# Optimization experiments

Measured on AMD Instinct MI355X. Metric: run time of the kernel, lower is better.

The kernel has to match this reference:

```python
import jax, jax.numpy as jnp
import numpy as np

H = 1024   # hidden_dim
V = 32000  # vocab_size
L = 256    # sequence length


def setup_inputs() -> dict:
    key = jax.random.key(0)
    ks = jax.random.split(key, 12)
    s = 0.02
    rn = lambda k, shape: jax.random.normal(k, shape, jnp.float32) * s
    return dict(
        input_seq=jax.random.randint(ks[0], (L,), 0, V),
        embeds=rn(ks[1], (V, H)),
        enc_Wih=rn(ks[2], (4 * H, H)), enc_Whh=rn(ks[3], (4 * H, H)),
        enc_bih=jnp.zeros(4 * H, jnp.float32), enc_bhh=jnp.zeros(4 * H, jnp.float32),
        dec_Wih=rn(ks[4], (4 * H, 2 * H)), dec_Whh=rn(ks[5], (4 * H, H)),
        dec_bih=jnp.zeros(4 * H, jnp.float32), dec_bhh=jnp.zeros(4 * H, jnp.float32),
        out_W=rn(ks[6], (V, H)), out_b=jnp.zeros(V, jnp.float32),
        v=jax.random.uniform(ks[7], (H,), jnp.float32) * 0.05,
        w1=jax.random.uniform(ks[8], (H, H), jnp.float32) * 0.05,
        w2=jax.random.uniform(ks[9], (H, H), jnp.float32) * 0.05,
    )


def _lstm_cell(x, h, c, Wih, Whh, bih, bhh):
    # PyTorch LSTM gate order: i, f, g, o
    g = Wih @ x + bih + Whh @ h + bhh
    i, f, gg, o = jnp.split(g, 4)
    i, f, o = jax.nn.sigmoid(i), jax.nn.sigmoid(f), jax.nn.sigmoid(o)
    c_new = f * c + i * jnp.tanh(gg)
    h_new = o * jnp.tanh(c_new)
    return h_new, c_new


def reference(input_seq, embeds, enc_Wih, enc_Whh, enc_bih, enc_bhh,
              dec_Wih, dec_Whh, dec_bih, dec_bhh, out_W, out_b, v, w1, w2):
    x_emb = embeds[input_seq]  # (L, H)

    # --- encoder LSTM (batch=1, seq-major) ---
    def enc_step(carry, x):
        h, c = carry
        h, c = _lstm_cell(x, h, c, enc_Wih, enc_Whh, enc_bih, enc_bhh)
        return (h, c), h

    h0 = jnp.zeros(H, jnp.float32)
    (h, c), E = jax.lax.scan(enc_step, (h0, h0), x_emb)  # E: (L, H)

    # additive attention: score_i = v . tanh(w1 @ h + w2 @ e_i)
    # precompute E @ w2^T once (same math as recomputing each step)
    Ew2 = E @ w2.T  # (L, H)

    def dec_step(carry, _):
        h, c, prev = carry
        prev_r = jax.nn.relu(prev)                       # relu on prev embedding
        scores = jnp.tanh(w1 @ h + Ew2) @ v              # (L,)
        a = jax.nn.softmax(scores)
        ctx = a @ E                                      # (H,)
        xin = jnp.concatenate([prev_r, ctx])             # (2H,)
        h2, c2 = _lstm_cell(xin, h, c, dec_Wih, dec_Whh, dec_bih, dec_bhh)
        logits = out_W @ h2 + out_b                      # (V,)
        idx = jnp.argmax(logits)
        return (h2, c2, embeds[idx]), (logits, idx)

    _, (preds, seq) = jax.lax.scan(dec_step, (h, c, jnp.zeros(H, jnp.float32)),
                                   None, length=L)
    return preds, seq  # (L, V) logits, (L,) predicted ids
```

## Files before the change

kernel.cpp:

```cpp
#include <hip/hip_runtime.h>
#include <math.h>


#define H   1024
#define V   32000
#define L   256
#define NB  256
#define NT  512
#define NW  (NT/64)
#define MARGIN 2e-4f

typedef unsigned long long u64;

__device__ __forceinline__ float wsum(float v){
  #pragma unroll
  for (int off = 32; off > 0; off >>= 1) v += __shfl_down(v, off, 64);
  return v;
}
__device__ __forceinline__ float wmaxf(float v){
  #pragma unroll
  for (int off = 32; off > 0; off >>= 1) v = fmaxf(v, __shfl_down(v, off, 64));
  return v;
}
__device__ __forceinline__ u64 wmaxu(u64 v){
  #pragma unroll
  for (int off = 32; off > 0; off >>= 1){
    u64 o = __shfl_down(v, off, 64);
    if (o > v) v = o;
  }
  return v;
}
__device__ __forceinline__ float sigmoidf(float x){ return 1.f/(1.f+expf(-x)); }
__device__ __forceinline__ unsigned fkey(float f){
  unsigned u = __float_as_uint(f);
  return (u & 0x80000000u) ? ~u : (u | 0x80000000u);
}
__device__ __forceinline__ float unfkey(unsigned k){
  unsigned u = (k & 0x80000000u) ? (k & 0x7FFFFFFFu) : ~k;
  return __uint_as_float(u);
}
__device__ __forceinline__ float dotp(const float* __restrict__ Wr,
                                      const float4* __restrict__ x4, int lane){
  const float4* w4 = (const float4*)Wr;
  float s = 0.f;
  #pragma unroll
  for (int u = 0; u < 4; ++u){
    float4 a = w4[lane + 64*u];
    float4 x = x4[lane + 64*u];
    s += a.x*x.x + a.y*x.y + a.z*x.z + a.w*x.w;
  }
  return s;
}
__device__ __forceinline__ float bdot8(uint4 q, float4 ha, float4 hb){
  float s;
  s  = __uint_as_float(q.x << 16)         * ha.x;
  s += __uint_as_float(q.x & 0xFFFF0000u) * ha.y;
  s += __uint_as_float(q.y << 16)         * ha.z;
  s += __uint_as_float(q.y & 0xFFFF0000u) * ha.w;
  s += __uint_as_float(q.z << 16)         * hb.x;
  s += __uint_as_float(q.z & 0xFFFF0000u) * hb.y;
  s += __uint_as_float(q.w << 16)         * hb.z;
  s += __uint_as_float(q.w & 0xFFFF0000u) * hb.w;
  return s;
}

__device__ __forceinline__ void ow_issue(const float* __restrict__ outW,
                                         int r0, int w, int lane, int g,
                                         float* dst){
  #pragma unroll
  for (int rr2 = 0; rr2 < 2; ++rr2){
    const int k  = w*16 + g*2 + rr2;
    const int kc = (k > 124) ? 124 : k;
    const float* src = outW + (size_t)(r0 + kc)*H + lane*4;
    #pragma unroll
    for (int kk = 0; kk < 4; ++kk){
      __builtin_amdgcn_global_load_lds(
          (const __attribute__((address_space(1))) unsigned int*)(src + kk*256),
          (__attribute__((address_space(3))) unsigned int*)(dst + rr2*H + kk*256),
          16, 0, 0);
    }
  }
}
__device__ __forceinline__ void owh_issue(const unsigned short* __restrict__ owbf,
                                          int r0, int w, int lane, int g,
                                          unsigned short* dst){
  #pragma unroll
  for (int rr2 = 0; rr2 < 2; ++rr2){
    const int k  = w*16 + g*2 + rr2;
    const int kc = (k > 124) ? 124 : k;
    const unsigned short* src = owbf + (size_t)(r0 + kc)*H + lane*8;
    #pragma unroll
    for (int kk = 0; kk < 2; ++kk){
      __builtin_amdgcn_global_load_lds(
          (const __attribute__((address_space(1))) unsigned int*)(src + kk*512),
          (__attribute__((address_space(3))) unsigned int*)(dst + rr2*1024 + kk*512),
          16, 0, 0);
    }
  }
}

__device__ __forceinline__ void pub(u64* ch, int idx, unsigned tag, float f){
  u64 v = ((u64)tag << 32) | (u64)__float_as_uint(f);
  __hip_atomic_store(ch + idx, v, __ATOMIC_RELAXED, __HIP_MEMORY_SCOPE_AGENT);
}
__device__ __forceinline__ float spin1(u64* p, unsigned tag){
  u64 v = __hip_atomic_load(p, __ATOMIC_RELAXED, __HIP_MEMORY_SCOPE_AGENT);
  while ((unsigned)(v >> 32) != tag){
    __builtin_amdgcn_s_sleep(2);
    v = __hip_atomic_load(p, __ATOMIC_RELAXED, __HIP_MEMORY_SCOPE_AGENT);
  }
  return __uint_as_float((unsigned)v);
}
__device__ __forceinline__ void ch_read(u64* ch, unsigned tag, float* dst, int tid){
  u64 v0 = __hip_atomic_load(ch + tid,      __ATOMIC_RELAXED, __HIP_MEMORY_SCOPE_AGENT);
  u64 v1 = __hip_atomic_load(ch + tid + NT, __ATOMIC_RELAXED, __HIP_MEMORY_SCOPE_AGENT);
  while ((unsigned)(v0 >> 32) != tag){
    __builtin_amdgcn_s_sleep(2);
    v0 = __hip_atomic_load(ch + tid, __ATOMIC_RELAXED, __HIP_MEMORY_SCOPE_AGENT);
  }
  while ((unsigned)(v1 >> 32) != tag){
    __builtin_amdgcn_s_sleep(2);
    v1 = __hip_atomic_load(ch + tid + NT, __ATOMIC_RELAXED, __HIP_MEMORY_SCOPE_AGENT);
  }
  dst[tid]      = __uint_as_float((unsigned)v0);
  dst[tid + NT] = __uint_as_float((unsigned)v1);
}
__device__ __forceinline__ unsigned win_reduce(u64* slot, unsigned tag,
                                               u64* s_k, unsigned* s_w,
                                               int tid, int w, int lane){
  u64 key = 0ull;
  if (tid < NB){
    u64* p = slot + tid;
    u64 v = __hip_atomic_load(p, __ATOMIC_RELAXED, __HIP_MEMORY_SCOPE_AGENT);
    while ((unsigned)(v >> 47) != tag){
      __builtin_amdgcn_s_sleep(2);
      v = __hip_atomic_load(p, __ATOMIC_RELAXED, __HIP_MEMORY_SCOPE_AGENT);
    }
    key = v & 0x7FFFFFFFFFFFull;
  }
  key = wmaxu(key);
  if (lane == 0) s_k[w] = key;
  __syncthreads();
  if (tid == 0){
    u64 m = s_k[0];
    for (int k = 1; k < NW; ++k) if (s_k[k] > m) m = s_k[k];
    *s_w = 0x7FFFu - (unsigned)(m & 0x7FFFull);
  }
  __syncthreads();
  return *s_w;
}

__device__ __forceinline__ unsigned resolve_winner(
    unsigned T, u64* chWinP, u64* chWin2,
    const float* __restrict__ outW, const float* sB,
    const float* s_logf, const float* s_ob,
    u64* s_wk, u64* s_k, float* s_bv, int* s_bi, u64* s_m12,
    int* s_nc, int* s_cr, unsigned* s_widx,
    int b, int tid, int w, int lane)
{
  const int pb = (int)(T & 1u);
  u64* pair = chWinP + pb*2*NB;
  {
    u64 v = __hip_atomic_load(pair + tid, __ATOMIC_RELAXED, __HIP_MEMORY_SCOPE_AGENT);
    while ((unsigned)(v >> 47) != T){
      __builtin_amdgcn_s_sleep(2);
      v = __hip_atomic_load(pair + tid, __ATOMIC_RELAXED, __HIP_MEMORY_SCOPE_AGENT);
    }
    s_wk[tid] = v & 0x7FFFFFFFFFFFull;
  }
  __syncthreads();
  u64 a = (tid < NB) ? s_wk[2*tid] : 0ull;
  a = wmaxu(a);
  if (lane == 0) s_k[w] = a;
  __syncthreads();
  if (tid == 0){
    u64 m = s_k[0];
    for (int k = 1; k < NW; ++k) if (s_k[k] > m) m = s_k[k];
    s_m12[0] = m;
  }
  __syncthreads();
  const u64 m1 = s_m12[0];
  const unsigned widx1 = 0x7FFFu - (unsigned)(m1 & 0x7FFFull);
  const int beta = (int)(widx1 / 125u);
  u64 c = (tid < NB) ? ((tid == beta) ? s_wk[2*tid+1] : s_wk[2*tid]) : 0ull;
  c = wmaxu(c);
  if (lane == 0) s_k[w] = c;
  __syncthreads();
  if (tid == 0){
    u64 m = s_k[0];
    for (int k = 1; k < NW; ++k) if (s_k[k] > m) m = s_k[k];
    s_m12[1] = m;
  }
  __syncthreads();
  const float f1 = unfkey((unsigned)(m1 >> 15));
  const float f2 = unfkey((unsigned)(s_m12[1] >> 15));
  if (f1 - f2 >= MARGIN) return widx1;

  if (tid == 0) *s_nc = 0;
  __syncthreads();
  const float thr = f1 - MARGIN;
  if (tid < 125 && s_logf[tid] >= thr){
    int sl = atomicAdd(s_nc, 1);
    if (sl < 16) s_cr[sl] = tid;
  }
  __syncthreads();
  const int nc = min(*s_nc, 16);
  float cv = -INFINITY; int ci = 0x7FFFFFFF;
  for (int q = w; q < nc; q += NW){
    const int lr = s_cr[q];
    float s = wsum(dotp(outW + (size_t)(b*125 + lr)*H, (const float4*)sB, lane));
    if (lane == 0){
      const float dv = s + s_ob[lr];
      const int gr = b*125 + lr;
      if (dv > cv || (dv == cv && gr < ci)){ cv = dv; ci = gr; }
    }
  }
  if (lane == 0){ s_bv[w] = cv; s_bi[w] = ci; }
  __syncthreads();
  if (tid == 0){
    float v0 = -INFINITY; int i0 = 0x7FFFFFFF;
    for (int k = 0; k < NW; ++k){
      if (s_bv[k] > v0 || (s_bv[k] == v0 && s_bi[k] < i0)){ v0 = s_bv[k]; i0 = s_bi[k]; }
    }
    const u64 pk = ((u64)T << 47) | ((u64)fkey(v0) << 15)
                 | (u64)(0x7FFFu - ((unsigned)i0 & 0x7FFFu));
    __hip_atomic_store(chWin2 + pb*NB + b, pk,
                       __ATOMIC_RELAXED, __HIP_MEMORY_SCOPE_AGENT);
  }
  __syncthreads();
  return win_reduce(chWin2 + pb*NB, T, s_k, s_widx, tid, w, lane);
}

__global__ __launch_bounds__(NT, 1) void seq2seq_fused_bf16(
    const int*   __restrict__ seq_in, const float* __restrict__ embeds,
    const float* __restrict__ eWih,   const float* __restrict__ eWhh,
    const float* __restrict__ ebih,   const float* __restrict__ ebhh,
    const float* __restrict__ dWih,   const float* __restrict__ dWhh,
    const float* __restrict__ dbih,   const float* __restrict__ dbhh,
    const float* __restrict__ outW,   const float* __restrict__ outb,
    const float* __restrict__ vvec,   const float* __restrict__ w1,
    const float* __restrict__ w2,
    float* __restrict__ out, u64* __restrict__ ws,
    const unsigned short* __restrict__ owbf)
{
  const int b = blockIdx.x, tid = threadIdx.x;
  const int w = tid >> 6, lane = tid & 63;
  const int j0 = b * 4;

  u64* chH  = ws;
  u64* chW1 = ws + 2*H;
  u64* chSc = ws + 4*H;
  u64* chCx = ws + 4*H + 2*NB;
  u64* chH2 = ws + 6*H + 2*NB;
  u64* chWinP = ws + 8*H + 2*NB;
  u64* chWin2 = ws + 8*H + 6*NB;

  __shared__ __align__(16) float sA[H];
  __shared__ __align__(16) float sB[H];
  __shared__ __align__(16) float sMyE[H];
  __shared__ __align__(16) float sEw2[H];
  __shared__ __align__(16) float sEcol[L*4];
  __shared__ __align__(16) unsigned short sOWh[NW][2][2048];
  __shared__ __align__(16) float sV[H];
  __shared__ __align__(16) u64 s_wk[NT];
  __shared__ float s_logf[128];
  __shared__ float s_ob[128];
  __shared__ float s_gate[16], s_gpart[16], s_c[4];
  __shared__ float s_redA[NW], s_red4[NW][4];
  __shared__ float s_bv[NW], s_bv2[NW];
  __shared__ int   s_bi[NW];
  __shared__ float s_bcast[2];
  __shared__ u64   s_k[NW];
  __shared__ u64   s_m12[2];
  __shared__ int   s_nc, s_cr[16];
  __shared__ unsigned s_widx;

  if (tid < 4) s_c[tid] = 0.f;
  for (int i = tid; i < H; i += NT) sV[i] = vvec[i];
  if (tid < 128) s_ob[tid] = outb[b*125 + ((tid > 124) ? 124 : tid)];

  for (int t = 0; t < L; ++t){
    if (t == 0){
      for (int i = tid; i < H; i += NT) sB[i] = 0.f;
    } else {
      ch_read(chH + (t & 1)*H, (unsigned)t, sB, tid);
    }
    if (t == b + 1){ sMyE[tid] = sB[tid]; sMyE[tid + NT] = sB[tid + NT]; }
    const int tok = seq_in[t];
    for (int i = tid; i < H; i += NT) sA[i] = embeds[(size_t)tok*H + i];
    __syncthreads();
    const float4* x4 = (const float4*)sA;
    const float4* h4 = (const float4*)sB;
    #pragma unroll
    for (int q2 = 0; q2 < 2; ++q2){
      const int lr = w + q2*NW;
      const int r  = (lr >> 2)*H + j0 + (lr & 3);
      float s = dotp(eWih + (size_t)r*H, x4, lane)
              + dotp(eWhh + (size_t)r*H, h4, lane);
      s = wsum(s);
      if (lane == 0) s_gate[lr] = s + ebih[r] + ebhh[r];
    }
    __syncthreads();
    if (tid < 4){
      const float ig = sigmoidf(s_gate[tid]);
      const float fg = sigmoidf(s_gate[4 + tid]);
      const float gg = tanhf   (s_gate[8 + tid]);
      const float og = sigmoidf(s_gate[12 + tid]);
      const float c  = fg*s_c[tid] + ig*gg;
      const float hn = og*tanhf(c);
      s_c[tid] = c;
      sEcol[t*4 + tid] = hn;
      pub(chH + ((t+1) & 1)*H, j0 + tid, (unsigned)(t+1), hn);
    }
  }
  if (b == L-1) ch_read(chH + ((L & 1))*H, (unsigned)L, sMyE, tid);
  __syncthreads();

  {
    const float4* e4p = (const float4*)sMyE;
    for (int g4 = 0; g4 < 32; ++g4){
      const int jr = w*128 + g4*4;
      const float4* W0 = (const float4*)(w2 + (size_t)(jr+0)*H);
      const float4* W1 = (const float4*)(w2 + (size_t)(jr+1)*H);
      const float4* W2 = (const float4*)(w2 + (size_t)(jr+2)*H);
      const float4* W3 = (const float4*)(w2 + (size_t)(jr+3)*H);
      float s0=0, s1=0, s2=0, s3=0;
      #pragma unroll
      for (int u = 0; u < 4; ++u){
        const float4 e = e4p[lane + 64*u];
        float4 a0 = W0[lane+64*u]; s0 += a0.x*e.x+a0.y*e.y+a0.z*e.z+a0.w*e.w;
        float4 a1 = W1[lane+64*u]; s1 += a1.x*e.x+a1.y*e.y+a1.z*e.z+a1.w*e.w;
        float4 a2 = W2[lane+64*u]; s2 += a2.x*e.x+a2.y*e.y+a2.z*e.z+a2.w*e.w;
        float4 a3 = W3[lane+64*u]; s3 += a3.x*e.x+a3.y*e.y+a3.z*e.z+a3.w*e.w;
      }
      s0 = wsum(s0); s1 = wsum(s1); s2 = wsum(s2); s3 = wsum(s3);
      if (lane == 0){ sEw2[jr]=s0; sEw2[jr+1]=s1; sEw2[jr+2]=s2; sEw2[jr+3]=s3; }
    }
  }
  __syncthreads();

  ch_read(chH + (L & 1)*H, (unsigned)L, sB, tid);
  __syncthreads();
  {
    const float4* hh4 = (const float4*)sB;
    #pragma unroll
    for (int q2 = 0; q2 < 2; ++q2){
      const int lr = w + q2*NW;
      const int r  = (lr >> 2)*H + j0 + (lr & 3);
      float s = wsum(dotp(dWhh + (size_t)r*H, hh4, lane));
      if (lane == 0) s_gpart[lr] = s + dbih[r] + dbhh[r];
    }
    if (w < 4){
      const int r = j0 + w;
      float s = wsum(dotp(w1 + (size_t)r*H, hh4, lane));
      if (lane == 0) pub(chW1 + 0*H, r, 1u, s);
    }
  }

  for (int t = 0; t < L; ++t){
    unsigned widx = 0u;
    if (t > 0){
      widx = resolve_winner((unsigned)t, chWinP, chWin2, outW, sB,
                            s_logf, s_ob, s_wk, s_k, s_bv, s_bi, s_m12,
                            &s_nc, s_cr, &s_widx, b, tid, w, lane);
      if (b == 0 && tid == 0)
        __builtin_nontemporal_store((float)widx, out + (size_t)L*V + (t-1));
      for (int i = tid; i < H; i += NT)
        sA[i] = fmaxf(embeds[(size_t)widx*H + i], 0.f);
      __syncthreads();
      const float4* pr4 = (const float4*)sA;
      #pragma unroll
      for (int q2 = 0; q2 < 2; ++q2){
        const int lr = w + q2*NW;
        const int r  = (lr >> 2)*H + j0 + (lr & 3);
        float s = wsum(dotp(dWih + (size_t)r*2*H, pr4, lane));
        if (lane == 0) s_gpart[lr] += s;
      }
    }
    owh_issue(owbf, b*125, w, lane, 0, &sOWh[w][0][0]);
    owh_issue(owbf, b*125, w, lane, 1, &sOWh[w][1][0]);

    __syncthreads();
    ch_read(chW1 + (t & 1)*H, (unsigned)(t+1), sA, tid);
    __syncthreads();
    {
      float p = 0.f;
      for (int i = tid; i < H; i += NT) p += sV[i]*tanhf(sA[i] + sEw2[i]);
      p = wsum(p);
      if (lane == 0) s_redA[w] = p;
      __syncthreads();
      if (tid == 0){
        float s = 0.f;
        for (int k = 0; k < NW; ++k) s += s_redA[k];
        pub(chSc + (t & 1)*NB, b, (unsigned)(t+1), s);
      }
    }

    __syncthreads();
    {
      float sv = -INFINITY;
      if (tid < L) sv = spin1(chSc + (t & 1)*NB + tid, (unsigned)(t+1));
      float mx = wmaxf(sv);
      if (lane == 0) s_redA[w] = mx;
      __syncthreads();
      if (tid == 0){
        float m = s_redA[0];
        for (int k = 1; k < NW; ++k) m = fmaxf(m, s_redA[k]);
        s_bcast[0] = m;
      }
      __syncthreads();
      const float m = s_bcast[0];
      float e = (tid < L) ? expf(sv - m) : 0.f;
      float ss = wsum(e);
      if (lane == 0) s_redA[w] = ss;
      __syncthreads();
      if (tid == 0){
        float s = 0.f;
        for (int k = 0; k < NW; ++k) s += s_redA[k];
        s_bcast[1] = s;
      }
      __syncthreads();
      const float a = e / s_bcast[1];
      float qx = 0, qy = 0, qz = 0, qw = 0;
      if (tid < L){
        const float4 ev = *(const float4*)(sEcol + tid*4);
        qx = a*ev.x; qy = a*ev.y; qz = a*ev.z; qw = a*ev.w;
      }
      qx = wsum(qx); qy = wsum(qy); qz = wsum(qz); qw = wsum(qw);
      if (lane == 0){ s_red4[w][0]=qx; s_red4[w][1]=qy; s_red4[w][2]=qz; s_red4[w][3]=qw; }
      __syncthreads();
      if (tid < 4){
        float s = 0.f;
        for (int k = 0; k < NW; ++k) s += s_red4[k][tid];
        pub(chCx + (t & 1)*H, j0 + tid, (unsigned)(t+1), s);
      }
    }

    ch_read(chCx + (t & 1)*H, (unsigned)(t+1), sA, tid);
    __syncthreads();
    const float4* cx4 = (const float4*)sA;
    #pragma unroll
    for (int q2 = 0; q2 < 2; ++q2){
      const int lr = w + q2*NW;
      const int r  = (lr >> 2)*H + j0 + (lr & 3);
      float s = wsum(dotp(dWih + (size_t)r*2*H + H, cx4, lane));
      if (lane == 0) s_gate[lr] = s_gpart[lr] + s;
    }
    __syncthreads();
    if (tid < 4){
      const float ig = sigmoidf(s_gate[tid]);
      const float fg = sigmoidf(s_gate[4 + tid]);
      const float gg = tanhf   (s_gate[8 + tid]);
      const float og = sigmoidf(s_gate[12 + tid]);
      const float c  = fg*s_c[tid] + ig*gg;
      const float hn = og*tanhf(c);
      s_c[tid] = c;
      pub(chH2 + ((t+1) & 1)*H, j0 + tid, (unsigned)(t+1), hn);
    }

    ch_read(chH2 + ((t+1) & 1)*H, (unsigned)(t+1), sB, tid);
    __syncthreads();
    {
      const float4* h4b = (const float4*)sB;
      const float4 hA0 = h4b[2*lane],     hA1 = h4b[2*lane+1];
      const float4 hB0 = h4b[128+2*lane], hB1 = h4b[128+2*lane+1];
      float bv1 = -INFINITY, bv2 = -INFINITY; int bi1 = 0x7FFFFFFF;
      const int r0 = b * 125;

#define EB_GROUP(G, WSTR)                                                      \
      {                                                                        \
        asm volatile("s_waitcnt vmcnt(" WSTR ")" ::: "memory");                \
        const uint4* rq = (const uint4*)&sOWh[w][(G)&1][0];                    \
        const uint4 q0 = rq[lane],     q1 = rq[lane+64];                       \
        const uint4 q2 = rq[lane+128], q3 = rq[lane+192];                      \
        float s0 = bdot8(q0, hA0, hA1) + bdot8(q1, hB0, hB1);                  \
        float s1 = bdot8(q2, hA0, hA1) + bdot8(q3, hB0, hB1);                  \
        if ((G) < 6) owh_issue(owbf, r0, w, lane, (G)+2, &sOWh[w][(G)&1][0]);  \
        s0 = wsum(s0); s1 = wsum(s1);                                          \
        if (lane == 0){                                                        \
          const int k0 = w*16 + (G)*2;                                         \
          const float d0 = s0 + s_ob[k0], d1 = s1 + s_ob[k0+1];                \
          s_logf[k0] = d0; s_logf[k0+1] = d1;                                  \
          if (k0 <= 124){                                                      \
            if (d0 > bv1 || (d0 == bv1 && r0+k0 < bi1)){ bv2=bv1; bv1=d0; bi1=r0+k0; } \
            else if (d0 > bv2) bv2 = d0;                                       \
          }                                                                    \
          if (k0+1 <= 124){                                                    \
            if (d1 > bv1 || (d1 == bv1 && r0+k0+1 < bi1)){ bv2=bv1; bv1=d1; bi1=r0+k0+1; } \
            else if (d1 > bv2) bv2 = d1;                                       \
          }                                                                    \
        }                                                                      \
      }

      EB_GROUP(0, "0")
      EB_GROUP(1, "4")
      EB_GROUP(2, "4")
      EB_GROUP(3, "4")
      EB_GROUP(4, "4")
      EB_GROUP(5, "4")
      EB_GROUP(6, "4")
      EB_GROUP(7, "0")
#undef EB_GROUP

      if (lane == 0){ s_bv[w] = bv1; s_bi[w] = bi1; s_bv2[w] = bv2; }
      __syncthreads();
      if (tid == 0){
        float v1 = -INFINITY, v2 = -INFINITY; int i1 = 0x7FFFFFFF, aw = 0;
        for (int k = 0; k < NW; ++k){
          if (s_bv[k] > v1 || (s_bv[k] == v1 && s_bi[k] < i1)){ v1 = s_bv[k]; i1 = s_bi[k]; aw = k; }
        }
        for (int k = 0; k < NW; ++k){
          const float cc = (k == aw) ? s_bv2[k] : s_bv[k];
          if (cc > v2) v2 = cc;
        }
        const u64 k1 = ((u64)(unsigned)(t+1) << 47) | ((u64)fkey(v1) << 15)
                     | (u64)(0x7FFFu - ((unsigned)i1 & 0x7FFFu));
        const u64 k2 = ((u64)(unsigned)(t+1) << 47) | ((u64)fkey(v2) << 15);
        u64* pr = chWinP + ((t+1) & 1)*2*NB + 2*b;
        __hip_atomic_store(pr,     k1, __ATOMIC_RELAXED, __HIP_MEMORY_SCOPE_AGENT);
        __hip_atomic_store(pr + 1, k2, __ATOMIC_RELAXED, __HIP_MEMORY_SCOPE_AGENT);
      }
      if (tid < 125)
        __builtin_nontemporal_store(s_logf[tid], out + (size_t)t*V + r0 + tid);

      const float4* hh4 = (const float4*)sB;
      if (w < 4){
        const int r = j0 + w;
        float s = wsum(dotp(w1 + (size_t)r*H, hh4, lane));
        if (lane == 0) pub(chW1 + ((t+1) & 1)*H, r, (unsigned)(t+2), s);
      }
      #pragma unroll
      for (int q2i = 0; q2i < 2; ++q2i){
        const int lr = w + q2i*NW;
        const int r  = (lr >> 2)*H + j0 + (lr & 3);
        float s = wsum(dotp(dWhh + (size_t)r*H, hh4, lane));
        if (lane == 0) s_gpart[lr] = s + dbih[r] + dbhh[r];
      }
    }
  }

  {
    unsigned widx = resolve_winner((unsigned)L, chWinP, chWin2, outW, sB,
                                   s_logf, s_ob, s_wk, s_k, s_bv, s_bi, s_m12,
                                   &s_nc, s_cr, &s_widx, b, tid, w, lane);
    if (b == 0 && tid == 0)
      __builtin_nontemporal_store((float)widx, out + (size_t)L*V + (L-1));
  }
}

__global__ __launch_bounds__(NT, 1) void seq2seq_fused_f32(
    const int*   __restrict__ seq_in, const float* __restrict__ embeds,
    const float* __restrict__ eWih,   const float* __restrict__ eWhh,
    const float* __restrict__ ebih,   const float* __restrict__ ebhh,
    const float* __restrict__ dWih,   const float* __restrict__ dWhh,
    const float* __restrict__ dbih,   const float* __restrict__ dbhh,
    const float* __restrict__ outW,   const float* __restrict__ outb,
    const float* __restrict__ vvec,   const float* __restrict__ w1,
    const float* __restrict__ w2,
    float* __restrict__ out, u64* __restrict__ ws)
{
  const int b = blockIdx.x, tid = threadIdx.x;
  const int w = tid >> 6, lane = tid & 63;
  const int j0 = b * 4;

  u64* chH  = ws;
  u64* chW1 = ws + 2*H;
  u64* chSc = ws + 4*H;
  u64* chCx = ws + 4*H + 2*NB;
  u64* chH2 = ws + 6*H + 2*NB;
  u64* chWin= ws + 8*H + 2*NB;

  __shared__ __align__(16) float sA[H];
  __shared__ __align__(16) float sB[H];
  __shared__ __align__(16) float sMyE[H];
  __shared__ __align__(16) float sEw2[H];
  __shared__ __align__(16) float sEcol[L*4];
  __shared__ __align__(16) float sOW[NW][2][2*H];
  __shared__ __align__(16) float sV[H];
  __shared__ float s_logf[128];
  __shared__ float s_ob[128];
  __shared__ float s_gate[16], s_gpart[16], s_c[4];
  __shared__ float s_redA[NW], s_red4[NW][4];
  __shared__ float s_bv[NW];
  __shared__ int   s_bi[NW];
  __shared__ float s_bcast[2];
  __shared__ u64   s_k[NW];
  __shared__ unsigned s_widx;

  if (tid < 4) s_c[tid] = 0.f;
  for (int i = tid; i < H; i += NT) sV[i] = vvec[i];
  if (tid < 128) s_ob[tid] = outb[b*125 + ((tid > 124) ? 124 : tid)];

  for (int t = 0; t < L; ++t){
    if (t == 0){
      for (int i = tid; i < H; i += NT) sB[i] = 0.f;
    } else {
      ch_read(chH + (t & 1)*H, (unsigned)t, sB, tid);
    }
    if (t == b + 1){ sMyE[tid] = sB[tid]; sMyE[tid + NT] = sB[tid + NT]; }
    const int tok = seq_in[t];
    for (int i = tid; i < H; i += NT) sA[i] = embeds[(size_t)tok*H + i];
    __syncthreads();
    const float4* x4 = (const float4*)sA;
    const float4* h4 = (const float4*)sB;
    #pragma unroll
    for (int q2 = 0; q2 < 2; ++q2){
      const int lr = w + q2*NW;
      const int r  = (lr >> 2)*H + j0 + (lr & 3);
      float s = dotp(eWih + (size_t)r*H, x4, lane)
              + dotp(eWhh + (size_t)r*H, h4, lane);
      s = wsum(s);
      if (lane == 0) s_gate[lr] = s + ebih[r] + ebhh[r];
    }
    __syncthreads();
    if (tid < 4){
      const float ig = sigmoidf(s_gate[tid]);
      const float fg = sigmoidf(s_gate[4 + tid]);
      const float gg = tanhf   (s_gate[8 + tid]);
      const float og = sigmoidf(s_gate[12 + tid]);
      const float c  = fg*s_c[tid] + ig*gg;
      const float hn = og*tanhf(c);
      s_c[tid] = c;
      sEcol[t*4 + tid] = hn;
      pub(chH + ((t+1) & 1)*H, j0 + tid, (unsigned)(t+1), hn);
    }
  }
  if (b == L-1) ch_read(chH + ((L & 1))*H, (unsigned)L, sMyE, tid);
  __syncthreads();

  {
    const float4* e4p = (const float4*)sMyE;
    for (int g4 = 0; g4 < 32; ++g4){
      const int jr = w*128 + g4*4;
      const float4* W0 = (const float4*)(w2 + (size_t)(jr+0)*H);
      const float4* W1 = (const float4*)(w2 + (size_t)(jr+1)*H);
      const float4* W2 = (const float4*)(w2 + (size_t)(jr+2)*H);
      const float4* W3 = (const float4*)(w2 + (size_t)(jr+3)*H);
      float s0=0, s1=0, s2=0, s3=0;
      #pragma unroll
      for (int u = 0; u < 4; ++u){
        const float4 e = e4p[lane + 64*u];
        float4 a0 = W0[lane+64*u]; s0 += a0.x*e.x+a0.y*e.y+a0.z*e.z+a0.w*e.w;
        float4 a1 = W1[lane+64*u]; s1 += a1.x*e.x+a1.y*e.y+a1.z*e.z+a1.w*e.w;
        float4 a2 = W2[lane+64*u]; s2 += a2.x*e.x+a2.y*e.y+a2.z*e.z+a2.w*e.w;
        float4 a3 = W3[lane+64*u]; s3 += a3.x*e.x+a3.y*e.y+a3.z*e.z+a3.w*e.w;
      }
      s0 = wsum(s0); s1 = wsum(s1); s2 = wsum(s2); s3 = wsum(s3);
      if (lane == 0){ sEw2[jr]=s0; sEw2[jr+1]=s1; sEw2[jr+2]=s2; sEw2[jr+3]=s3; }
    }
  }
  __syncthreads();

  for (int t = 0; t < L; ++t){
    unsigned widx = 0u;
    if (t > 0){
      widx = win_reduce(chWin + ((t-1) & 1)*NB, (unsigned)t, s_k, &s_widx, tid, w, lane);
      if (b == 0 && tid == 0) out[(size_t)L*V + (t-1)] = (float)widx;
    }
    if (t == 0) ch_read(chH + ((L & 1))*H, (unsigned)L, sB, tid);
    for (int i = tid; i < H; i += NT){
      float pv = (t > 0) ? embeds[(size_t)widx*H + i] : 0.f;
      sA[i] = fmaxf(pv, 0.f);
    }
    __syncthreads();
    const float4* hh4 = (const float4*)sB;
    const float4* pr4 = (const float4*)sA;
    #pragma unroll
    for (int q2 = 0; q2 < 2; ++q2){
      const int lr = w + q2*NW;
      const int r  = (lr >> 2)*H + j0 + (lr & 3);
      float s = dotp(dWhh + (size_t)r*H, hh4, lane);
      if (t > 0) s += dotp(dWih + (size_t)r*2*H, pr4, lane);
      s = wsum(s);
      if (lane == 0) s_gpart[lr] = s + dbih[r] + dbhh[r];
    }
    if (w < 4){
      const int r = j0 + w;
      float s = wsum(dotp(w1 + (size_t)r*H, hh4, lane));
      if (lane == 0) pub(chW1 + (t & 1)*H, r, (unsigned)(t+1), s);
    }
    ow_issue(outW, b*125, w, lane, 0, &sOW[w][0][0]);
    ow_issue(outW, b*125, w, lane, 1, &sOW[w][1][0]);

    __syncthreads();
    ch_read(chW1 + (t & 1)*H, (unsigned)(t+1), sA, tid);
    __syncthreads();
    {
      float p = 0.f;
      for (int i = tid; i < H; i += NT) p += sV[i]*tanhf(sA[i] + sEw2[i]);
      p = wsum(p);
      if (lane == 0) s_redA[w] = p;
      __syncthreads();
      if (tid == 0){
        float s = 0.f;
        for (int k = 0; k < NW; ++k) s += s_redA[k];
        pub(chSc + (t & 1)*NB, b, (unsigned)(t+1), s);
      }
    }

// ... 181 lines not shown
```

Measured before the change: 9.455 ms.

## Warp-specialize decoder: split output-projection waves from recurrent hop waves

Splits each block's 8 waves into 4 'hop' waves that run the attention and LSTM recurrence chain and 4 waves that stream the bf16 output projection and the per-block argmax. The two groups communicate through LDS ready counters and a custom partial barrier instead of __syncthreads. The goal is to take the 32000-row vocab projection off the serial critical path: the winner resolution for step t is deferred until after the next step's attention and context work, overlapping the logits computation with that recurrence. In exchange it adds shared-memory double buffers, spin-waits inside the block and halves the waves available to each role, with risk of ordering bugs.

```diff
diff --git a/kernel.cpp b/kernel.cpp
--- a/kernel.cpp
+++ b/kernel.cpp
@@ -8,6 +8,7 @@
 #define NB  256
 #define NT  512
 #define NW  (NT/64)
+#define NHOP 4
 #define MARGIN 2e-4f
 
 typedef unsigned long long u64;
@@ -81,49 +82,75 @@
     }
   }
 }
-__device__ __forceinline__ void owh_issue(const unsigned short* __restrict__ owbf,
-                                          int r0, int w, int lane, int g,
-                                          unsigned short* dst){
+__device__ __forceinline__ void owh2_issue(const unsigned short* __restrict__ owbf,
+                                           int r0, int we, int lane, int g,
+                                           unsigned short* dst){
   #pragma unroll
-  for (int rr2 = 0; rr2 < 2; ++rr2){
-    const int k  = w*16 + g*2 + rr2;
+  for (int rr = 0; rr < 2; ++rr){
+    const int k  = we*32 + g*2 + rr;
     const int kc = (k > 124) ? 124 : k;
     const unsigned short* src = owbf + (size_t)(r0 + kc)*H + lane*8;
     #pragma unroll
     for (int kk = 0; kk < 2; ++kk){
       __builtin_amdgcn_global_load_lds(
           (const __attribute__((address_space(1))) unsigned int*)(src + kk*512),
-          (__attribute__((address_space(3))) unsigned int*)(dst + rr2*1024 + kk*512),
+          (__attribute__((address_space(3))) unsigned int*)(dst + rr*1024 + kk*512),
           16, 0, 0);
     }
   }
 }
 
+__device__ __forceinline__ u64 aload(u64* p){
+  return __hip_atomic_load(p, __ATOMIC_RELAXED, __HIP_MEMORY_SCOPE_AGENT);
+}
 __device__ __forceinline__ void pub(u64* ch, int idx, unsigned tag, float f){
   u64 v = ((u64)tag << 32) | (u64)__float_as_uint(f);
   __hip_atomic_store(ch + idx, v, __ATOMIC_RELAXED, __HIP_MEMORY_SCOPE_AGENT);
 }
 __device__ __forceinline__ float spin1(u64* p, unsigned tag){
-  u64 v = __hip_atomic_load(p, __ATOMIC_RELAXED, __HIP_MEMORY_SCOPE_AGENT);
+  u64 v = aload(p);
   while ((unsigned)(v >> 32) != tag){
     __builtin_amdgcn_s_sleep(2);
-    v = __hip_atomic_load(p, __ATOMIC_RELAXED, __HIP_MEMORY_SCOPE_AGENT);
+    v = aload(p);
   }
   return __uint_as_float((unsigned)v);
 }
+__device__ __forceinline__ u64 spin47(u64* p, unsigned tag){
+  u64 v = aload(p);
+  while ((unsigned)(v >> 47) != tag){
+    __builtin_amdgcn_s_sleep(2);
+    v = aload(p);
+  }
+  return v;
+}
 __device__ __forceinline__ void ch_read(u64* ch, unsigned tag, float* dst, int tid){
-  u64 v0 = __hip_atomic_load(ch + tid,      __ATOMIC_RELAXED, __HIP_MEMORY_SCOPE_AGENT);
-  u64 v1 = __hip_atomic_load(ch + tid + NT, __ATOMIC_RELAXED, __HIP_MEMORY_SCOPE_AGENT);
-  while ((unsigned)(v0 >> 32) != tag){
-    __builtin_amdgcn_s_sleep(2);
-    v0 = __hip_atomic_load(ch + tid, __ATOMIC_RELAXED, __HIP_MEMORY_SCOPE_AGENT);
-  }
-  while ((unsigned)(v1 >> 32) != tag){
-    __builtin_amdgcn_s_sleep(2);
-    v1 = __hip_atomic_load(ch + tid + NT, __ATOMIC_RELAXED, __HIP_MEMORY_SCOPE_AGENT);
-  }
+  u64 v0 = aload(ch + tid);
+  u64 v1 = aload(ch + tid + NT);
+  while ((unsigned)(v0 >> 32) != tag){ __builtin_amdgcn_s_sleep(2); v0 = aload(ch + tid); }
+  while ((unsigned)(v1 >> 32) != tag){ __builtin_amdgcn_s_sleep(2); v1 = aload(ch + tid + NT); }
   dst[tid]      = __uint_as_float((unsigned)v0);
   dst[tid + NT] = __uint_as_float((unsigned)v1);
+}
+__device__ __forceinline__ void ch_read4(u64* ch, unsigned tag, float* dst, int tid){
+  u64 v[4];
+  #pragma unroll
+  for (int k = 0; k < 4; ++k) v[k] = aload(ch + tid + k*256);
+  #pragma unroll
+  for (int k = 0; k < 4; ++k){
+    while ((unsigned)(v[k] >> 32) != tag){
+      __builtin_amdgcn_s_sleep(2);
+      v[k] = aload(ch + tid + k*256);
+    }
+  }
+  #pragma unroll
+  for (int k = 0; k < 4; ++k) dst[tid + k*256] = __uint_as_float((unsigned)v[k]);
+}
+__device__ __forceinline__ void hbar(int* c, int& ep, int lane){
+  ep += NHOP;
+  if (lane == 0)
+    __hip_atomic_fetch_add(c, 1, __ATOMIC_RELEASE, __HIP_MEMORY_SCOPE_WORKGROUP);
+  while (__hip_atomic_load(c, __ATOMIC_ACQUIRE, __HIP_MEMORY_SCOPE_WORKGROUP) < ep)
+    __builtin_amdgcn_s_sleep(1);
 }
 __device__ __forceinline__ unsigned win_reduce(u64* slot, unsigned tag,
                                                u64* s_k, unsigned* s_w,
@@ -131,11 +158,8 @@
   u64 key = 0ull;
   if (tid < NB){
     u64* p = slot + tid;
-    u64 v = __hip_atomic_load(p, __ATOMIC_RELAXED, __HIP_MEMORY_SCOPE_AGENT);
-    while ((unsigned)(v >> 47) != tag){
-      __builtin_amdgcn_s_sleep(2);
-      v = __hip_atomic_load(p, __ATOMIC_RELAXED, __HIP_MEMORY_SCOPE_AGENT);
-    }
+    u64 v = aload(p);
+    while ((unsigned)(v >> 47) != tag){ __builtin_amdgcn_s_sleep(2); v = aload(p); }
     key = v & 0x7FFFFFFFFFFFull;
   }
   key = wmaxu(key);
@@ -148,87 +172,6 @@
   }
   __syncthreads();
   return *s_w;
-}
-
-__device__ __forceinline__ unsigned resolve_winner(
-    unsigned T, u64* chWinP, u64* chWin2,
-    const float* __restrict__ outW, const float* sB,
-    const float* s_logf, const float* s_ob,
-    u64* s_wk, u64* s_k, float* s_bv, int* s_bi, u64* s_m12,
-    int* s_nc, int* s_cr, unsigned* s_widx,
-    int b, int tid, int w, int lane)
-{
-  const int pb = (int)(T & 1u);
-  u64* pair = chWinP + pb*2*NB;
-  {
-    u64 v = __hip_atomic_load(pair + tid, __ATOMIC_RELAXED, __HIP_MEMORY_SCOPE_AGENT);
-    while ((unsigned)(v >> 47) != T){
-      __builtin_amdgcn_s_sleep(2);
-      v = __hip_atomic_load(pair + tid, __ATOMIC_RELAXED, __HIP_MEMORY_SCOPE_AGENT);
-    }
-    s_wk[tid] = v & 0x7FFFFFFFFFFFull;
-  }
-  __syncthreads();
-  u64 a = (tid < NB) ? s_wk[2*tid] : 0ull;
-  a = wmaxu(a);
-  if (lane == 0) s_k[w] = a;
-  __syncthreads();
-  if (tid == 0){
-    u64 m = s_k[0];
-    for (int k = 1; k < NW; ++k) if (s_k[k] > m) m = s_k[k];
-    s_m12[0] = m;
-  }
-  __syncthreads();
-  const u64 m1 = s_m12[0];
-  const unsigned widx1 = 0x7FFFu - (unsigned)(m1 & 0x7FFFull);
-  const int beta = (int)(widx1 / 125u);
-  u64 c = (tid < NB) ? ((tid == beta) ? s_wk[2*tid+1] : s_wk[2*tid]) : 0ull;
-  c = wmaxu(c);
-  if (lane == 0) s_k[w] = c;
-  __syncthreads();
-  if (tid == 0){
-    u64 m = s_k[0];
-    for (int k = 1; k < NW; ++k) if (s_k[k] > m) m = s_k[k];
-    s_m12[1] = m;
-  }
-  __syncthreads();
-  const float f1 = unfkey((unsigned)(m1 >> 15));
-  const float f2 = unfkey((unsigned)(s_m12[1] >> 15));
-  if (f1 - f2 >= MARGIN) return widx1;
-
-  if (tid == 0) *s_nc = 0;
-  __syncthreads();
-  const float thr = f1 - MARGIN;
-  if (tid < 125 && s_logf[tid] >= thr){
-    int sl = atomicAdd(s_nc, 1);
-    if (sl < 16) s_cr[sl] = tid;
-  }
-  __syncthreads();
-  const int nc = min(*s_nc, 16);
-  float cv = -INFINITY; int ci = 0x7FFFFFFF;
-  for (int q = w; q < nc; q += NW){
-    const int lr = s_cr[q];
-    float s = wsum(dotp(outW + (size_t)(b*125 + lr)*H, (const float4*)sB, lane));
-    if (lane == 0){
-      const float dv = s + s_ob[lr];
-      const int gr = b*125 + lr;
-      if (dv > cv || (dv == cv && gr < ci)){ cv = dv; ci = gr; }
-    }
-  }
-  if (lane == 0){ s_bv[w] = cv; s_bi[w] = ci; }
-  __syncthreads();
-  if (tid == 0){
-    float v0 = -INFINITY; int i0 = 0x7FFFFFFF;
-    for (int k = 0; k < NW; ++k){
-      if (s_bv[k] > v0 || (s_bv[k] == v0 && s_bi[k] < i0)){ v0 = s_bv[k]; i0 = s_bi[k]; }
-    }
-    const u64 pk = ((u64)T << 47) | ((u64)fkey(v0) << 15)
-                 | (u64)(0x7FFFu - ((unsigned)i0 & 0x7FFFu));
-    __hip_atomic_store(chWin2 + pb*NB + b, pk,
-                       __ATOMIC_RELAXED, __HIP_MEMORY_SCOPE_AGENT);
-  }
-  __syncthreads();
-  return win_reduce(chWin2 + pb*NB, T, s_k, s_widx, tid, w, lane);
 }
 
 __global__ __launch_bounds__(NT, 1) void seq2seq_fused_bf16(
@@ -247,11 +190,11 @@
   const int w = tid >> 6, lane = tid & 63;
   const int j0 = b * 4;
 
-  u64* chH  = ws;
-  u64* chW1 = ws + 2*H;
-  u64* chSc = ws + 4*H;
-  u64* chCx = ws + 4*H + 2*NB;
-  u64* chH2 = ws + 6*H + 2*NB;
+  u64* chH    = ws;
+  u64* chW1   = ws + 2*H;
+  u64* chSc   = ws + 4*H;
+  u64* chCx   = ws + 4*H + 2*NB;
+  u64* chH2   = ws + 6*H + 2*NB;
   u64* chWinP = ws + 8*H + 2*NB;
   u64* chWin2 = ws + 8*H + 6*NB;
 
@@ -260,22 +203,28 @@
   __shared__ __align__(16) float sMyE[H];
   __shared__ __align__(16) float sEw2[H];
   __shared__ __align__(16) float sEcol[L*4];
-  __shared__ __align__(16) unsigned short sOWh[NW][2][2048];
+  __shared__ __align__(16) unsigned short sOWh[4][2][2048];
   __shared__ __align__(16) float sV[H];
-  __shared__ __align__(16) u64 s_wk[NT];
+  __shared__ __align__(16) float sH2[2][H];
+  __shared__ __align__(16) float sCtx[H];
+  __shared__ __align__(16) float sPr[H];
   __shared__ float s_logf[128];
   __shared__ float s_ob[128];
   __shared__ float s_gate[16], s_gpart[16], s_c[4];
-  __shared__ float s_redA[NW], s_red4[NW][4];
-  __shared__ float s_bv[NW], s_bv2[NW];
-  __shared__ int   s_bi[NW];
-  __shared__ float s_bcast[2];
-  __shared__ u64   s_k[NW];
-  __shared__ u64   s_m12[2];
+  __shared__ float s_redA[8], s_red4[8][4];
+  __shared__ float s_bv[8];
+  __shared__ int   s_bi[8];
+  __shared__ float s_ebv1[4], s_ebv2[4];
+  __shared__ int   s_ebi[4];
+  __shared__ int   s_ewdone[4];
+  __shared__ int   s_h2rdy;
+  __shared__ int   s_hb;
+  __shared__ u64   s_k[8];
   __shared__ int   s_nc, s_cr[16];
-  __shared__ unsigned s_widx;
 
   if (tid < 4) s_c[tid] = 0.f;
+  if (tid < 4) s_ewdone[tid] = 0;
+  if (tid == 0){ s_h2rdy = 0; s_hb = 0; }
   for (int i = tid; i < H; i += NT) sV[i] = vvec[i];
   if (tid < 128) s_ob[tid] = outb[b*125 + ((tid > 124) ? 124 : tid)];
 
@@ -339,10 +288,10 @@
   }
   __syncthreads();
 
-  ch_read(chH + (L & 1)*H, (unsigned)L, sB, tid);
+  ch_read(chH + (L & 1)*H, (unsigned)L, sH2[0], tid);
   __syncthreads();
   {
-    const float4* hh4 = (const float4*)sB;
+    const float4* hh4 = (const float4*)sH2[0];
     #pragma unroll
     for (int q2 = 0; q2 < 2; ++q2){
       const int lr = w + q2*NW;
@@ -356,129 +305,34 @@
       if (lane == 0) pub(chW1 + 0*H, r, 1u, s);
     }
   }
-
-  for (int t = 0; t < L; ++t){
-    unsigned widx = 0u;
-    if (t > 0){
-      widx = resolve_winner((unsigned)t, chWinP, chWin2, outW, sB,
-                            s_logf, s_ob, s_wk, s_k, s_bv, s_bi, s_m12,
-                            &s_nc, s_cr, &s_widx, b, tid, w, lane);
-      if (b == 0 && tid == 0)
-        __builtin_nontemporal_store((float)widx, out + (size_t)L*V + (t-1));
-      for (int i = tid; i < H; i += NT)
-        sA[i] = fmaxf(embeds[(size_t)widx*H + i], 0.f);
-      __syncthreads();
-      const float4* pr4 = (const float4*)sA;
-      #pragma unroll
-      for (int q2 = 0; q2 < 2; ++q2){
-        const int lr = w + q2*NW;
-        const int r  = (lr >> 2)*H + j0 + (lr & 3);
-        float s = wsum(dotp(dWih + (size_t)r*2*H, pr4, lane));
-        if (lane == 0) s_gpart[lr] += s;
-      }
-    }
-    owh_issue(owbf, b*125, w, lane, 0, &sOWh[w][0][0]);
-    owh_issue(owbf, b*125, w, lane, 1, &sOWh[w][1][0]);
-
-    __syncthreads();
-    ch_read(chW1 + (t & 1)*H, (unsigned)(t+1), sA, tid);
-    __syncthreads();
-    {
-      float p = 0.f;
-      for (int i = tid; i < H; i += NT) p += sV[i]*tanhf(sA[i] + sEw2[i]);
-      p = wsum(p);
-      if (lane == 0) s_redA[w] = p;
-      __syncthreads();
-      if (tid == 0){
-        float s = 0.f;
-        for (int k = 0; k < NW; ++k) s += s_redA[k];
-        pub(chSc + (t & 1)*NB, b, (unsigned)(t+1), s);
-      }
-    }
-
-    __syncthreads();
-    {
-      float sv = -INFINITY;
-      if (tid < L) sv = spin1(chSc + (t & 1)*NB + tid, (unsigned)(t+1));
-      float mx = wmaxf(sv);
-      if (lane == 0) s_redA[w] = mx;
-      __syncthreads();
-      if (tid == 0){
-        float m = s_redA[0];
-        for (int k = 1; k < NW; ++k) m = fmaxf(m, s_redA[k]);
-        s_bcast[0] = m;
-      }
-      __syncthreads();
-      const float m = s_bcast[0];
-      float e = (tid < L) ? expf(sv - m) : 0.f;
-      float ss = wsum(e);
-      if (lane == 0) s_redA[w] = ss;
-      __syncthreads();
-      if (tid == 0){
-        float s = 0.f;
-        for (int k = 0; k < NW; ++k) s += s_redA[k];
-        s_bcast[1] = s;
-      }
-      __syncthreads();
-      const float a = e / s_bcast[1];
-      float qx = 0, qy = 0, qz = 0, qw = 0;
-      if (tid < L){
-        const float4 ev = *(const float4*)(sEcol + tid*4);
-        qx = a*ev.x; qy = a*ev.y; qz = a*ev.z; qw = a*ev.w;
-      }
-      qx = wsum(qx); qy = wsum(qy); qz = wsum(qz); qw = wsum(qw);
-      if (lane == 0){ s_red4[w][0]=qx; s_red4[w][1]=qy; s_red4[w][2]=qz; s_red4[w][3]=qw; }
-      __syncthreads();
-      if (tid < 4){
-        float s = 0.f;
-        for (int k = 0; k < NW; ++k) s += s_red4[k][tid];
-        pub(chCx + (t & 1)*H, j0 + tid, (unsigned)(t+1), s);
-      }
-    }
-
-    ch_read(chCx + (t & 1)*H, (unsigned)(t+1), sA, tid);
-    __syncthreads();
-    const float4* cx4 = (const float4*)sA;
-    #pragma unroll
-    for (int q2 = 0; q2 < 2; ++q2){
-      const int lr = w + q2*NW;
-      const int r  = (lr >> 2)*H + j0 + (lr & 3);
-      float s = wsum(dotp(dWih + (size_t)r*2*H + H, cx4, lane));
-      if (lane == 0) s_gate[lr] = s_gpart[lr] + s;
-    }
-    __syncthreads();
-    if (tid < 4){
-      const float ig = sigmoidf(s_gate[tid]);
-      const float fg = sigmoidf(s_gate[4 + tid]);
-      const float gg = tanhf   (s_gate[8 + tid]);
-      const float og = sigmoidf(s_gate[12 + tid]);
-      const float c  = fg*s_c[tid] + ig*gg;
-      const float hn = og*tanhf(c);
-      s_c[tid] = c;
-      pub(chH2 + ((t+1) & 1)*H, j0 + tid, (unsigned)(t+1), hn);
-    }
-
-    ch_read(chH2 + ((t+1) & 1)*H, (unsigned)(t+1), sB, tid);
-    __syncthreads();
-    {
-      const float4* h4b = (const float4*)sB;
+  __syncthreads();
+
+  if (w >= NHOP){
+    const int we = w - NHOP;
+    const int r0 = b * 125;
+    owh2_issue(owbf, r0, we, lane, 0, &sOWh[we][0][0]);
+    owh2_issue(owbf, r0, we, lane, 1, &sOWh[we][1][0]);
+    volatile int* rdy = &s_h2rdy;
+    for (int s = 0; s < L; ++s){
+      while (*rdy < s + 1) __builtin_amdgcn_s_sleep(2);
+      __builtin_amdgcn_sched_barrier(0);
+      const float4* h4b = (const float4*)sH2[(s+1)&1];
       const float4 hA0 = h4b[2*lane],     hA1 = h4b[2*lane+1];
       const float4 hB0 = h4b[128+2*lane], hB1 = h4b[128+2*lane+1];
       float bv1 = -INFINITY, bv2 = -INFINITY; int bi1 = 0x7FFFFFFF;
-      const int r0 = b * 125;
-
-#define EB_GROUP(G, WSTR)                                                      \
+
+#define EG(G)                                                                  \
       {                                                                        \
-        asm volatile("s_waitcnt vmcnt(" WSTR ")" ::: "memory");                \
-        const uint4* rq = (const uint4*)&sOWh[w][(G)&1][0];                    \
-        const uint4 q0 = rq[lane],     q1 = rq[lane+64];                       \
-        const uint4 q2 = rq[lane+128], q3 = rq[lane+192];                      \
-        float s0 = bdot8(q0, hA0, hA1) + bdot8(q1, hB0, hB1);                  \
-        float s1 = bdot8(q2, hA0, hA1) + bdot8(q3, hB0, hB1);                  \
-        if ((G) < 6) owh_issue(owbf, r0, w, lane, (G)+2, &sOWh[w][(G)&1][0]);  \
+        asm volatile("s_waitcnt vmcnt(4)" ::: "memory");                       \
+        const uint4* rq = (const uint4*)&sOWh[we][(G)&1][0];                   \
+        const uint4 qa = rq[lane],     qb = rq[lane+64];                       \
+        const uint4 qc = rq[lane+128], qd = rq[lane+192];                      \
+        float s0 = bdot8(qa, hA0, hA1) + bdot8(qb, hB0, hB1);                  \
+        float s1 = bdot8(qc, hA0, hA1) + bdot8(qd, hB0, hB1);                  \
+        owh2_issue(owbf, r0, we, lane, ((G)+2)&15, &sOWh[we][(G)&1][0]);       \
         s0 = wsum(s0); s1 = wsum(s1);                                          \
         if (lane == 0){                                                        \
-          const int k0 = w*16 + (G)*2;                                         \
+          const int k0 = we*32 + (G)*2;                                        \
           const float d0 = s0 + s_ob[k0], d1 = s1 + s_ob[k0+1];                \
           s_logf[k0] = d0; s_logf[k0+1] = d1;                                  \
           if (k0 <= 124){                                                      \
@@ -491,60 +345,240 @@
           }                                                                    \
         }                                                                      \
       }
-
-      EB_GROUP(0, "0")
-      EB_GROUP(1, "4")
-      EB_GROUP(2, "4")
-      EB_GROUP(3, "4")
-      EB_GROUP(4, "4")
-      EB_GROUP(5, "4")
-      EB_GROUP(6, "4")
-      EB_GROUP(7, "0")
-#undef EB_GROUP
-
-      if (lane == 0){ s_bv[w] = bv1; s_bi[w] = bi1; s_bv2[w] = bv2; }
-      __syncthreads();
+      EG(0)  EG(1)  EG(2)  EG(3)  EG(4)  EG(5)  EG(6)  EG(7)
+      EG(8)  EG(9)  EG(10) EG(11) EG(12) EG(13) EG(14) EG(15)
+#undef EG
+      if (lane == 0){
+        s_ebv1[we] = bv1; s_ebv2[we] = bv2; s_ebi[we] = bi1;
+        asm volatile("s_waitcnt lgkmcnt(0)" ::: "memory");
+        *(volatile int*)&s_ewdone[we] = s + 1;
+      }
+    }
+    asm volatile("s_waitcnt vmcnt(0)" ::: "memory");
+  } else {
+    const int hw = w;
+    int ep = 0;
+
+    auto W_phase = [&](int t) -> unsigned {
+      volatile int* ed = s_ewdone;
+      while (ed[0] < t || ed[1] < t || ed[2] < t || ed[3] < t)
+        __builtin_amdgcn_s_sleep(2);
+      __builtin_amdgcn_sched_barrier(0);
       if (tid == 0){
         float v1 = -INFINITY, v2 = -INFINITY; int i1 = 0x7FFFFFFF, aw = 0;
-        for (int k = 0; k < NW; ++k){
-          if (s_bv[k] > v1 || (s_bv[k] == v1 && s_bi[k] < i1)){ v1 = s_bv[k]; i1 = s_bi[k]; aw = k; }
-        }
-        for (int k = 0; k < NW; ++k){
-          const float cc = (k == aw) ? s_bv2[k] : s_bv[k];
+        for (int k = 0; k < 4; ++k){
+          if (s_ebv1[k] > v1 || (s_ebv1[k] == v1 && s_ebi[k] < i1)){
+            v1 = s_ebv1[k]; i1 = s_ebi[k]; aw = k;
+          }
+        }
+        for (int k = 0; k < 4; ++k){
+          const float cc = (k == aw) ? s_ebv2[k] : s_ebv1[k];
           if (cc > v2) v2 = cc;
         }
-        const u64 k1 = ((u64)(unsigned)(t+1) << 47) | ((u64)fkey(v1) << 15)
+        const u64 k1 = ((u64)(unsigned)t << 47) | ((u64)fkey(v1) << 15)
                      | (u64)(0x7FFFu - ((unsigned)i1 & 0x7FFFu));
-        const u64 k2 = ((u64)(unsigned)(t+1) << 47) | ((u64)fkey(v2) << 15);
-        u64* pr = chWinP + ((t+1) & 1)*2*NB + 2*b;
+        const u64 k2 = ((u64)(unsigned)t << 47) | ((u64)fkey(v2) << 15);
+        u64* pr = chWinP + (t & 1)*2*NB + 2*b;
         __hip_atomic_store(pr,     k1, __ATOMIC_RELAXED, __HIP_MEMORY_SCOPE_AGENT);
         __hip_atomic_store(pr + 1, k2, __ATOMIC_RELAXED, __HIP_MEMORY_SCOPE_AGENT);
       }
+      u64* pair = chWinP + (t & 1)*2*NB;
+      const u64 vb = spin47(pair + 2*tid,     (unsigned)t);
+      const u64 vs = spin47(pair + 2*tid + 1, (unsigned)t);
+      const u64 best = vb & 0x7FFFFFFFFFFFull, second = vs & 0x7FFFFFFFFFFFull;
+      u64 a1 = wmaxu(best);
+      if (lane == 0) s_k[hw] = a1;
+      hbar(&s_hb, ep, lane);
+      u64 m1 = s_k[0];
+      for (int k = 1; k < 4; ++k) if (s_k[k] > m1) m1 = s_k[k];
+      const unsigned widx1 = 0x7FFFu - (unsigned)(m1 & 0x7FFFull);
+      const int beta = (int)(widx1 / 125u);
+      u64 c = (tid == beta) ? second : best;
+      c = wmaxu(c);
+      if (lane == 0) s_k[4 + hw] = c;
+      hbar(&s_hb, ep, lane);
+      u64 m2 = s_k[4];
+      for (int k = 5; k < 8; ++k) if (s_k[k] > m2) m2 = s_k[k];
+      const float f1 = unfkey((unsigned)(m1 >> 15));
+      const float f2 = unfkey((unsigned)(m2 >> 15));
+      unsigned widx;
+      if (f1 - f2 >= MARGIN){
+        widx = widx1;
+      } else {
+        if (tid == 0) s_nc = 0;
+        hbar(&s_hb, ep, lane);
+        const float thr = f1 - MARGIN;
+        if (tid < 125 && s_logf[tid] >= thr){
+          int sl = __hip_atomic_fetch_add(&s_nc, 1, __ATOMIC_RELAXED,
+                                          __HIP_MEMORY_SCOPE_WORKGROUP);
+          if (sl < 16) s_cr[sl] = tid;
+        }
+        hbar(&s_hb, ep, lane);
+        const int nc = min(s_nc, 16);
+        float cv = -INFINITY; int ci = 0x7FFFFFFF;
+        const float4* h2c = (const float4*)sH2[t & 1];
+        for (int q = hw; q < nc; q += NHOP){
+          const int lr = s_cr[q];
+          float s = wsum(dotp(outW + (size_t)(b*125 + lr)*H, h2c, lane));
+          if (lane == 0){
+            const float dv = s + s_ob[lr];
+            const int gr = b*125 + lr;
+            if (dv > cv || (dv == cv && gr < ci)){ cv = dv; ci = gr; }
+          }
+        }
+        if (lane == 0){ s_bv[hw] = cv; s_bi[hw] = ci; }
+        hbar(&s_hb, ep, lane);
+        if (tid == 0){
+          float v0 = -INFINITY; int i0 = 0x7FFFFFFF;
+          for (int k = 0; k < 4; ++k){
+            if (s_bv[k] > v0 || (s_bv[k] == v0 && s_bi[k] < i0)){
+              v0 = s_bv[k]; i0 = s_bi[k];
+            }
+          }
+          const u64 pk = ((u64)(unsigned)t << 47) | ((u64)fkey(v0) << 15)
+                       | (u64)(0x7FFFu - ((unsigned)i0 & 0x7FFFu));
+          __hip_atomic_store(chWin2 + (t & 1)*NB + b, pk,
+                             __ATOMIC_RELAXED, __HIP_MEMORY_SCOPE_AGENT);
+        }
+        u64 key = spin47(chWin2 + (t & 1)*NB + tid, (unsigned)t) & 0x7FFFFFFFFFFFull;
+        key = wmaxu(key);
+        if (lane == 0) s_k[hw] = key;
+        hbar(&s_hb, ep, lane);
+        u64 mm = s_k[0];
+        for (int k = 1; k < 4; ++k) if (s_k[k] > mm) mm = s_k[k];
+        widx = 0x7FFFu - (unsigned)(mm & 0x7FFFull);
+      }
+      if (b == 0 && tid == 0)
+        __builtin_nontemporal_store((float)widx, out + (size_t)L*V + (t-1));
       if (tid < 125)
-        __builtin_nontemporal_store(s_logf[tid], out + (size_t)t*V + r0 + tid);
-
-      const float4* hh4 = (const float4*)sB;
-      if (w < 4){
-        const int r = j0 + w;
-        float s = wsum(dotp(w1 + (size_t)r*H, hh4, lane));
-        if (lane == 0) pub(chW1 + ((t+1) & 1)*H, r, (unsigned)(t+2), s);
-      }
-      #pragma unroll
-      for (int q2i = 0; q2i < 2; ++q2i){
-        const int lr = w + q2i*NW;
-        const int r  = (lr >> 2)*H + j0 + (lr & 3);
-        float s = wsum(dotp(dWhh + (size_t)r*H, hh4, lane));
-        if (lane == 0) s_gpart[lr] = s + dbih[r] + dbhh[r];
-      }
-    }
-  }
-
-  {
-    unsigned widx = resolve_winner((unsigned)L, chWinP, chWin2, outW, sB,
-                                   s_logf, s_ob, s_wk, s_k, s_bv, s_bi, s_m12,
-                                   &s_nc, s_cr, &s_widx, b, tid, w, lane);
-    if (b == 0 && tid == 0)
-      __builtin_nontemporal_store((float)widx, out + (size_t)L*V + (L-1));
+        __builtin_nontemporal_store(s_logf[tid],
+                                    out + (size_t)(t-1)*V + b*125 + tid);
+      return widx;
+    };
+
+    for (int t = 0; t < L; ++t){
+      {
+        u64* ch = chW1 + (t & 1)*H;
+        u64 v[4];
+        #pragma unroll
+        for (int k = 0; k < 4; ++k) v[k] = aload(ch + tid + k*256);
+        #pragma unroll
+        for (int k = 0; k < 4; ++k){
+          while ((unsigned)(v[k] >> 32) != (unsigned)(t+1)){
+            __builtin_amdgcn_s_sleep(2);
+            v[k] = aload(ch + tid + k*256);
+          }
+        }
+        float p = 0.f;
+        #pragma unroll
+        for (int k = 0; k < 4; ++k){
+          const int i = tid + k*256;
+          p += sV[i]*tanhf(__uint_as_float((unsigned)v[k]) + sEw2[i]);
+        }
+        p = wsum(p);
+        if (lane == 0) s_redA[hw] = p;
+        hbar(&s_hb, ep, lane);
+        if (tid == 0){
+          float s = s_redA[0]+s_redA[1]+s_redA[2]+s_redA[3];
+          pub(chSc + (t & 1)*NB, b, (unsigned)(t+1), s);
+        }
+        hbar(&s_hb, ep, lane);
+      }
+      {
+        const float sv = spin1(chSc + (t & 1)*NB + tid, (unsigned)(t+1));
+        float mx = wmaxf(sv);
+        if (lane == 0) s_redA[hw] = mx;
+        hbar(&s_hb, ep, lane);
+        const float m = fmaxf(fmaxf(s_redA[0], s_redA[1]),
+                              fmaxf(s_redA[2], s_redA[3]));
+        const float e = expf(sv - m);
+        float ss = wsum(e);
+        if (lane == 0) s_redA[4 + hw] = ss;
+        hbar(&s_hb, ep, lane);
+        const float sum = s_redA[4]+s_redA[5]+s_redA[6]+s_redA[7];
+        const float a = e / sum;
+        const float4 ev = *(const float4*)(sEcol + tid*4);
+        float qx = a*ev.x, qy = a*ev.y, qz = a*ev.z, qw = a*ev.w;
+        qx = wsum(qx); qy = wsum(qy); qz = wsum(qz); qw = wsum(qw);
+        if (lane == 0){
+          s_red4[hw][0]=qx; s_red4[hw][1]=qy; s_red4[hw][2]=qz; s_red4[hw][3]=qw;
+        }
+        hbar(&s_hb, ep, lane);
+        if (tid < 4){
+          float s = s_red4[0][tid]+s_red4[1][tid]+s_red4[2][tid]+s_red4[3][tid];
+          pub(chCx + (t & 1)*H, j0 + tid, (unsigned)(t+1), s);
+        }
+      }
+      if (t > 0){
+        const unsigned widx = W_phase(t);
+        {
+          const float4 evv = *(const float4*)(embeds + (size_t)widx*H + tid*4);
+          float4 rv;
+          rv.x = fmaxf(evv.x, 0.f); rv.y = fmaxf(evv.y, 0.f);
+          rv.z = fmaxf(evv.z, 0.f); rv.w = fmaxf(evv.w, 0.f);
+          *(float4*)(sPr + tid*4) = rv;
+        }
+        hbar(&s_hb, ep, lane);
+        const float4* pr4 = (const float4*)sPr;
+        float acc[4];
+        #pragma unroll
+        for (int i = 0; i < 4; ++i)
+          acc[i] = dotp(dWih + (size_t)(hw*H + j0 + i)*2*H, pr4, lane);
+        #pragma unroll
+        for (int i = 0; i < 4; ++i){
+          float s = wsum(acc[i]);
+          if (lane == 0) s_gpart[hw*4 + i] += s;
+        }
+      }
+      {
+        ch_read4(chCx + (t & 1)*H, (unsigned)(t+1), sCtx, tid);
+        hbar(&s_hb, ep, lane);
+        const float4* cx4 = (const float4*)sCtx;
+        float acc[4];
+        #pragma unroll
+        for (int i = 0; i < 4; ++i)
+          acc[i] = dotp(dWih + (size_t)(hw*H + j0 + i)*2*H + H, cx4, lane);
+        #pragma unroll
+        for (int i = 0; i < 4; ++i){
+          float s = wsum(acc[i]);
+          if (lane == 0) s_gate[hw*4 + i] = s_gpart[hw*4 + i] + s;
+        }
+        hbar(&s_hb, ep, lane);
+        if (tid < 4){
+          const float ig = sigmoidf(s_gate[tid]);
+          const float fg = sigmoidf(s_gate[4 + tid]);
+          const float gg = tanhf   (s_gate[8 + tid]);
+          const float og = sigmoidf(s_gate[12 + tid]);
+          const float c  = fg*s_c[tid] + ig*gg;
+          const float hn = og*tanhf(c);
+          s_c[tid] = c;
+          pub(chH2 + ((t+1) & 1)*H, j0 + tid, (unsigned)(t+1), hn);
+        }
+      }
+      {
+        ch_read4(chH2 + ((t+1) & 1)*H, (unsigned)(t+1), sH2[(t+1)&1], tid);
+        hbar(&s_hb, ep, lane);
+        if (tid == 0)
+          __hip_atomic_store(&s_h2rdy, t+1, __ATOMIC_RELEASE,
+                             __HIP_MEMORY_SCOPE_WORKGROUP);
+        const float4* hh4 = (const float4*)sH2[(t+1)&1];
+        {
+          float s = wsum(dotp(w1 + (size_t)(j0 + hw)*H, hh4, lane));
+          if (lane == 0) pub(chW1 + ((t+1) & 1)*H, j0 + hw, (unsigned)(t+2), s);
+        }
+        float acc[4];
+        #pragma unroll
+        for (int i = 0; i < 4; ++i)
+          acc[i] = dotp(dWhh + (size_t)(hw*H + j0 + i)*H, hh4, lane);
+        #pragma unroll
+        for (int i = 0; i < 4; ++i){
+          float s = wsum(acc[i]);
+          if (lane == 0)
+            s_gpart[hw*4 + i] = s + dbih[hw*H + j0 + i] + dbhh[hw*H + j0 + i];
+        }
+      }
+    }
+    (void)W_phase(L);
   }
 }
 
```

After: 9.055 ms. -4.2%, faster.
